# Kernel tuning notes

Hardware: AMD Instinct MI355X
Metric: run time of the kernel (lower is better)

Reference implementation:

```python
import jax, jax.numpy as jnp
import numpy as np

EPS = 1e-5


def _conv(x, w, b=None, pad=0):
    y = jax.lax.conv_general_dilated(
        x, w, window_strides=(1, 1), padding=[(pad, pad), (pad, pad)],
        dimension_numbers=('NCHW', 'OIHW', 'NCHW'))
    if b is not None:
        y = y + b[None, :, None, None]
    return y


def _bn(x, g, b, m, v):
    # eval-mode BatchNorm2d with running stats
    scale = (g / jnp.sqrt(v + EPS))[None, :, None, None]
    return (x - m[None, :, None, None]) * scale + b[None, :, None, None]


def setup_inputs() -> dict:
    key = jax.random.key(0)
    B, Ci, Cg, H, W = 4, 128, 64, 128, 128
    ks = iter(jax.random.split(key, 32))
    n = lambda shape, s=1.0: jax.random.normal(next(ks), shape, jnp.float32) * s
    return {
        'input': n((B, Ci, H, W)),
        'weight': n((B, Cg, H, W)),
        # conv11: 3x3, bias (norm_cfg=None) + ReLU
        'w11': n((Ci, Ci + Cg, 3, 3), 0.05), 'b11': n((Ci,), 0.05),
        # conv12: 1x1 -> Ci*9 per-pixel kernel generator
        'w12': n((Ci * 9, Ci, 1, 1), 0.05), 'b12': n((Ci * 9,), 0.05),
        # conv21: 3x3, bias + ReLU
        'w21': n((Ci, Ci + Cg, 3, 3), 0.05), 'b21': n((Ci,), 0.05),
        # conv22: 1x1 -> Ci*Ci channel-mix generator
        'w22': n((Ci * Ci, Ci, 1, 1), 0.05), 'b22': n((Ci * Ci,), 0.05),
        # BN after guided conv (self.local)
        'g1': 1.0 + n((Ci,), 0.1), 'be1': n((Ci,), 0.1), 'm1': n((Ci,), 0.1), 'v1': jnp.ones((Ci,), jnp.float32),
        # BN in self.br
        'g2': 1.0 + n((Ci,), 0.1), 'be2': n((Ci,), 0.1), 'm2': n((Ci,), 0.1), 'v2': jnp.ones((Ci,), jnp.float32),
        # conv3: 3x3 no bias (ConvModule with norm) + BN + ReLU
        'w3': n((Ci, Ci, 3, 3), 0.05),
        'g3': 1.0 + n((Ci,), 0.1), 'be3': n((Ci,), 0.1), 'm3': n((Ci,), 0.1), 'v3': jnp.ones((Ci,), jnp.float32),
    }


def _forward(input, weight, w11, b11, w12, b12, w21, b21, w22, b22,
             g1, be1, m1, v1, g2, be2, m2, v2, w3, g3, be3, m3, v3):
    B, Ci, H, W = input.shape
    wcat = jnp.concatenate([input, weight], axis=1)              # [B, Ci+Cg, H, W]
    w11o = jax.nn.relu(_conv(wcat, w11, b11, pad=1))             # [B, Ci, H, W]
    w12o = _conv(w11o, w12, b12, pad=0)                          # [B, Ci*9, H, W]
    w21o = jax.nn.relu(_conv(wcat, w21, b21, pad=1))             # [B, Ci, H, W]
    pooled = jnp.mean(w21o, axis=(2, 3), keepdims=True)          # [B, Ci, 1, 1]
    w22o = _conv(pooled, w22, b22, pad=0).reshape(B, Ci, Ci)     # [B, Ci, Ci]
    # Conv2dGuided: per-pixel 3x3 kernels from w12o applied depthwise
    xp = jnp.pad(input, ((0, 0), (0, 0), (1, 1), (1, 1)))
    patches = jnp.stack([xp[:, :, i:i + H, j:j + W]
                         for i in range(3) for j in range(3)], axis=2)  # [B, Ci, 9, H, W]
    local = jnp.sum(patches * w12o.reshape(B, Ci, 9, H, W), axis=2)     # [B, Ci, H, W]
    local = jax.nn.relu(_bn(local, g1, be1, m1, v1)).reshape(B, Ci, H * W)
    out = jnp.einsum('bij,bjn->bin', w22o, local).reshape(B, Ci, H, W)  # channel-mix bmm
    out = jax.nn.relu(_bn(out, g2, be2, m2, v2))                        # self.br
    out = jax.nn.relu(_bn(_conv(out, w3, None, pad=1), g3, be3, m3, v3))  # conv3
    return out


def reference(input, weight, w11, b11, w12, b12, w21, b21, w22, b22,
              g1, be1, m1, v1, g2, be2, m2, v2, w3, g3, be3, m3, v3):
    return _forward(input, weight, w11, b11, w12, b12, w21, b21, w22, b22,
                    g1, be1, m1, v1, g2, be2, m2, v2, w3, g3, be3, m3, v3)
```

## Files before the change

kernel.cpp:

```cpp
#include <hip/hip_runtime.h>
#include <math.h>

#define BB   4
#define CI   128
#define CG   64
#define CIN  192
#define HH   128
#define WW   128
#define PP   16384
#define EPSN 1e-5f

typedef unsigned short u16;
typedef unsigned int   u32;
typedef __attribute__((ext_vector_type(8))) short bf16x8;
typedef __attribute__((ext_vector_type(4))) float f32x4;

__device__ __forceinline__ u16 f2bf(float x) {
    union { float f; u32 u; } a; a.f = x;
    u32 u = a.u;
    return (u16)((u + 0x7FFFu + ((u >> 16) & 1u)) >> 16);
}
__device__ __forceinline__ float bf2f(u16 h) {
    union { u32 u; float f; } a; a.u = ((u32)h) << 16; return a.f;
}
__device__ __forceinline__ u32 swz(u32 o) { return o ^ ((o >> 4) & 0x70u); }

__device__ __forceinline__ void gld_lds16(const void* g, void* l) {
    __builtin_amdgcn_global_load_lds(
        (const __attribute__((address_space(1))) void*)g,
        (__attribute__((address_space(3))) void*)l, 16, 0, 0);
}

__global__ __launch_bounds__(256) void k_pack(
    const float* __restrict__ src0, int nch0,
    const float* __restrict__ src1, int nch1,
    u16* __restrict__ dhi, u16* __restrict__ dlo, int cinp)
{
    const int rr = blockIdx.x;
    const int b  = blockIdx.y;
    const int t  = threadIdx.x;
    u16* rh = dhi + ((size_t)b * 130 + rr) * 130 * cinp;
    u16* rl = dlo + ((size_t)b * 130 + rr) * 130 * cinp;

    if (rr == 0 || rr == 129) {
        u32* rh4 = (u32*)rh; u32* rl4 = (u32*)rl;
        const int tot = 130 * cinp / 2;
        for (int i = t; i < tot; i += 256) { rh4[i] = 0u; rl4[i] = 0u; }
        return;
    }
    const int y = rr - 1;
    for (int i = t; i < cinp; i += 256) {
        rh[i] = 0; rl[i] = 0;
        rh[129 * cinp + i] = 0; rl[129 * cinp + i] = 0;
    }

    __shared__ float xs[32][129];
    for (int ck = 0; ck < cinp / 32; ++ck) {
        __syncthreads();
        for (int i = t; i < 32 * 128; i += 256) {
            const int ch = i >> 7, col = i & 127;
            const int c = ck * 32 + ch;
            const float* sp = (c < nch0)
                ? src0 + ((size_t)b * nch0 + c) * PP
                : src1 + ((size_t)b * nch1 + (c - nch0)) * PP;
            xs[ch][col] = sp[y * WW + col];
        }
        __syncthreads();
        for (int i = t; i < 512; i += 256) {
            const int col = i >> 2, oct = i & 3;
            u16 hh[8], ll[8];
#pragma unroll
            for (int j = 0; j < 8; ++j) {
                const float v = xs[oct * 8 + j][col];
                const u16 h = f2bf(v);
                hh[j] = h; ll[j] = f2bf(v - bf2f(h));
            }
            const size_t off = (size_t)(col + 1) * cinp + ck * 32 + oct * 8;
            uint4 vh, vl;
            vh.x = (u32)hh[0] | ((u32)hh[1] << 16); vh.y = (u32)hh[2] | ((u32)hh[3] << 16);
            vh.z = (u32)hh[4] | ((u32)hh[5] << 16); vh.w = (u32)hh[6] | ((u32)hh[7] << 16);
            vl.x = (u32)ll[0] | ((u32)ll[1] << 16); vl.y = (u32)ll[2] | ((u32)ll[3] << 16);
            vl.z = (u32)ll[4] | ((u32)ll[5] << 16); vl.w = (u32)ll[6] | ((u32)ll[7] << 16);
            *(uint4*)(rh + off) = vh;
            *(uint4*)(rl + off) = vl;
        }
    }
}

__global__ __launch_bounds__(256) void k_wpack(
    const float* __restrict__ w0, const float* __restrict__ w1,
    u16* __restrict__ dst, int nmb, int nck, int cin)
{
    const int total = nmb * nck * 9 * 128 * 4;
    const int idx = blockIdx.x * 256 + threadIdx.x;
    if (idx >= total) return;
    const int oct = idx & 3; int r2 = idx >> 2;
    const int oc = r2 & 127; r2 >>= 7;
    const int tap = r2 % 9; r2 /= 9;
    const int ck = r2 % nck; r2 /= nck;
    const int mb = r2;
    const float* w = mb ? w1 : w0;
    u16 hh[8], ll[8];
#pragma unroll
    for (int j = 0; j < 8; ++j) {
        const int c = ck * 32 + oct * 8 + j;
        const float v = w[((size_t)oc * cin + c) * 9 + tap];
        const u16 h = f2bf(v);
        hh[j] = h; ll[j] = f2bf(v - bf2f(h));
    }
    const size_t halfs = (size_t)nmb * nck * 9 * 128 * 32;
    const size_t base = ((((size_t)mb * nck + ck) * 9 + tap) * 128 + oc) * 32 + oct * 8;
    uint4 vh, vl;
    vh.x = (u32)hh[0] | ((u32)hh[1] << 16); vh.y = (u32)hh[2] | ((u32)hh[3] << 16);
    vh.z = (u32)hh[4] | ((u32)hh[5] << 16); vh.w = (u32)hh[6] | ((u32)hh[7] << 16);
    vl.x = (u32)ll[0] | ((u32)ll[1] << 16); vl.y = (u32)ll[2] | ((u32)ll[3] << 16);
    vl.z = (u32)ll[4] | ((u32)ll[5] << 16); vl.w = (u32)ll[6] | ((u32)ll[7] << 16);
    *(uint4*)(dst + base) = vh;
    *(uint4*)(dst + halfs + base) = vl;
}

__global__ __launch_bounds__(256) void k_wpack12(
    const float* __restrict__ w12, u16* __restrict__ dst)
{
    const int idx = blockIdx.x * 256 + threadIdx.x;
    if (idx >= 18432) return;
    const int oct = idx & 15;
    const int g   = idx >> 4;
    const int cc  = g / 9, tap = g % 9;
    u16 hh[8], ll[8];
#pragma unroll
    for (int j = 0; j < 8; ++j) {
        const float v = w12[(size_t)g * 128 + oct * 8 + j];
        const u16 h = f2bf(v);
        hh[j] = h; ll[j] = f2bf(v - bf2f(h));
    }
    const size_t base = ((size_t)(tap * 128 + cc)) * 128 + oct * 8;
    uint4 vh, vl;
    vh.x = (u32)hh[0] | ((u32)hh[1] << 16); vh.y = (u32)hh[2] | ((u32)hh[3] << 16);
    vh.z = (u32)hh[4] | ((u32)hh[5] << 16); vh.w = (u32)hh[6] | ((u32)hh[7] << 16);
    vl.x = (u32)ll[0] | ((u32)ll[1] << 16); vl.y = (u32)ll[2] | ((u32)ll[3] << 16);
    vl.z = (u32)ll[4] | ((u32)ll[5] << 16); vl.w = (u32)ll[6] | ((u32)ll[7] << 16);
    *(uint4*)(dst + base) = vh;
    *(uint4*)(dst + 147456 + base) = vl;
}

template<int NCK, bool DUAL>
__global__ __launch_bounds__(256, 2) void k_conv_mfma(
    const u16* __restrict__ xhi, const u16* __restrict__ xlo,
    const u16* __restrict__ wA,
    const float* __restrict__ bias0, const float* __restrict__ bias1,
    const float* __restrict__ bng, const float* __restrict__ bnb,
    const float* __restrict__ bnm, const float* __restrict__ bnv,
    float* __restrict__ dst0, float* __restrict__ dst1,
    u16* __restrict__ y1ph, u16* __restrict__ y1pl)
{
    constexpr int CINP  = NCK * 32;
    constexpr int MBT   = DUAL ? 2 : 1;
    constexpr size_t WHALF = (size_t)MBT * NCK * 9 * 128 * 32;

    __shared__ char smem[73728];
    u16 (*Xs)[3][144][32] = (u16(*)[3][144][32])smem;
    u16 (*As)[128][32]    = (u16(*)[128][32])(smem + 55296);

    const int t    = threadIdx.x;
    const int wave = t >> 6;
    const int lane = t & 63;
    const int wm   = wave >> 1, wn = wave & 1;
    const int y    = blockIdx.x;
    const int mb   = blockIdx.y;
    const int b    = blockIdx.z;
    const int l15  = lane & 15;
    const int kg   = lane >> 4;

    f32x4 acc[4][4];
    if (DUAL) {
        const float* bp = mb ? bias1 : bias0;
#pragma unroll
        for (int fm = 0; fm < 4; ++fm) {
            const int ocb = wm * 64 + fm * 16 + kg * 4;
#pragma unroll
            for (int j = 0; j < 4; ++j) {
                const float bv = bp[ocb + j];
#pragma unroll
                for (int fn = 0; fn < 4; ++fn) acc[fm][fn][j] = bv;
            }
        }
    } else {
#pragma unroll
        for (int fm = 0; fm < 4; ++fm)
#pragma unroll
            for (int fn = 0; fn < 4; ++fn)
#pragma unroll
                for (int j = 0; j < 4; ++j) acc[fm][fn][j] = 0.0f;
    }

    const size_t xrow = (size_t)130 * CINP;

    for (int ck = 0; ck < NCK; ++ck) {
        __syncthreads();
        for (int idx = wave; idx < 54; idx += 4) {
            const int h = idx / 27, rem = idx % 27;
            const int r = rem / 9, iss = rem % 9;
            const u16* gb = (h ? xlo : xhi)
                + ((size_t)b * 130 + (y + r)) * xrow + ck * 32;
            const int o  = iss * 1024 + lane * 16;
            const int cc = o >> 6, rb = o & 63;
            gld_lds16((const char*)gb + (size_t)cc * (CINP * 2) + rb,
                      ((char*)&Xs[h][r][0][0]) + iss * 1024);
        }
        for (int tap = 0; tap < 9; ++tap) {
            for (int idx = wave; idx < 16; idx += 4) {
                const int h = idx >> 3, iss = idx & 7;
                const u16* gb = wA + (size_t)h * WHALF
                    + ((((size_t)mb * NCK + ck) * 9 + tap) * 128 * 32);
                gld_lds16((const char*)gb + iss * 1024 + lane * 16,
                          ((char*)&As[h][0][0]) + iss * 1024);
            }
            asm volatile("s_waitcnt vmcnt(0)" ::: "memory");
            __syncthreads();

            const int dy = tap / 3, dx = tap % 3;
            bf16x8 ah[4], al[4], bh[4], bl[4];
#pragma unroll
            for (int f = 0; f < 4; ++f) {
                const int row = wm * 64 + f * 16 + l15;
                ah[f] = *(const bf16x8*)&As[0][row][kg * 8];
                al[f] = *(const bf16x8*)&As[1][row][kg * 8];
                const int cc = wn * 64 + f * 16 + l15 + dx;
                bh[f] = *(const bf16x8*)&Xs[0][dy][cc][kg * 8];
                bl[f] = *(const bf16x8*)&Xs[1][dy][cc][kg * 8];
            }
#pragma unroll
            for (int fm = 0; fm < 4; ++fm)
#pragma unroll
                for (int fn = 0; fn < 4; ++fn) {
                    acc[fm][fn] = __builtin_amdgcn_mfma_f32_16x16x32_bf16(
                        al[fm], bh[fn], acc[fm][fn], 0, 0, 0);
                    acc[fm][fn] = __builtin_amdgcn_mfma_f32_16x16x32_bf16(
                        ah[fm], bl[fn], acc[fm][fn], 0, 0, 0);
                    acc[fm][fn] = __builtin_amdgcn_mfma_f32_16x16x32_bf16(
                        ah[fm], bh[fn], acc[fm][fn], 0, 0, 0);
                }
            __syncthreads();
        }
    }

    if (DUAL && mb == 0) {
        u16* img = (u16*)smem;
#pragma unroll
        for (int fm = 0; fm < 4; ++fm)
#pragma unroll
            for (int fn = 0; fn < 4; ++fn) {
                const int px = wn * 64 + fn * 16 + l15;
                const int c0 = wm * 64 + fm * 16 + kg * 4;
                u16 hh[4], ll[4];
#pragma unroll
                for (int j = 0; j < 4; ++j) {
                    const float v = fmaxf(acc[fm][fn][j], 0.0f);
                    const u16 h = f2bf(v);
                    hh[j] = h; ll[j] = f2bf(v - bf2f(h));
                }
                const u32 off = swz((u32)(px * 256 + c0 * 2));
                uint2 vh, vl;
                vh.x = (u32)hh[0] | ((u32)hh[1] << 16); vh.y = (u32)hh[2] | ((u32)hh[3] << 16);
                vl.x = (u32)ll[0] | ((u32)ll[1] << 16); vl.y = (u32)ll[2] | ((u32)ll[3] << 16);
                *(uint2*)((char*)img + off)         = vh;
                *(uint2*)((char*)img + 32768 + off) = vl;
            }
        __syncthreads();
        for (int h = 0; h < 2; ++h) {
            uint4* gd = (uint4*)((h ? y1pl : y1ph) + ((size_t)b * 128 + y) * 16384);
            const uint4* s4 = (const uint4*)(smem + h * 32768);
            for (int i = t; i < 2048; i += 256) gd[i] = s4[i];
        }
        return;
    }

    float* dst = DUAL ? dst1 : dst0;
#pragma unroll
    for (int fm = 0; fm < 4; ++fm) {
#pragma unroll
        for (int j = 0; j < 4; ++j) {
            const int oc = wm * 64 + fm * 16 + kg * 4 + j;
            float sc = 1.0f, sh = 0.0f;
            if (!DUAL) {
                sc = bng[oc] * rsqrtf(bnv[oc] + EPSN);
                sh = bnb[oc] - bnm[oc] * sc;
            }
            const size_t obase = ((size_t)b * CI + oc) * PP + (size_t)y * WW;
#pragma unroll
            for (int fn = 0; fn < 4; ++fn) {
                const int px = wn * 64 + fn * 16 + l15;
                float v = acc[fm][fn][j];
                if (!DUAL) v = fmaf(v, sc, sh);
                dst[obase + px] = fmaxf(v, 0.0f);
            }
        }
    }
}

__global__ __launch_bounds__(256) void k_pool(
    const float* __restrict__ y2, float* __restrict__ pooled)
{
    const int c = blockIdx.x, b = blockIdx.y, t = threadIdx.x;
    const float* src = y2 + ((size_t)b * CI + c) * PP;
    float s = 0.0f;
    for (int i = t; i < PP; i += 256) s += src[i];
    __shared__ float red[256];
    red[t] = s;
    __syncthreads();
    for (int st = 128; st > 0; st >>= 1) {
        if (t < st) red[t] += red[t + st];
        __syncthreads();
    }
    if (t == 0) pooled[b * CI + c] = red[0] * (1.0f / PP);
}

__global__ __launch_bounds__(256) void k_w22(
    const float* __restrict__ w22, const float* __restrict__ b22,
    const float* __restrict__ pooled, u16* __restrict__ w22p)
{
    const int b = blockIdx.y;
    const int o = blockIdx.x * 256 + threadIdx.x;
    __shared__ float pl[CI];
    if (threadIdx.x < CI) pl[threadIdx.x] = pooled[b * CI + threadIdx.x];
    __syncthreads();
    const float4* wr = (const float4*)(w22 + (size_t)o * CI);
    float acc = b22[o];
#pragma unroll 8
    for (int c4 = 0; c4 < CI / 4; ++c4) {
        const float4 w = wr[c4];
        acc += w.x * pl[c4 * 4 + 0] + w.y * pl[c4 * 4 + 1] +
               w.z * pl[c4 * 4 + 2] + w.w * pl[c4 * 4 + 3];
    }
    const u16 h = f2bf(acc);
    w22p[(size_t)b * 16384 + o] = h;
    w22p[65536 + (size_t)b * 16384 + o] = f2bf(acc - bf2f(h));
}

__global__ __launch_bounds__(256, 2) void k_guided_mfma(
    const float* __restrict__ input,
    const u16* __restrict__ y1p,
    const u16* __restrict__ w12p,
    const float* __restrict__ b12,
    const float* __restrict__ g1, const float* __restrict__ be1,
    const float* __restrict__ m1, const float* __restrict__ v1,
    u16* __restrict__ locp)
{
    __shared__ char smem[65536];
    const int t = threadIdx.x;
    const int wave = t >> 6, lane = t & 63;
    const int wm = wave >> 1, wn = wave & 1;
    const int l15 = lane & 15, kg = lane >> 4;
    const int y = blockIdx.x, b = blockIdx.y;

    for (int h = 0; h < 2; ++h) {
        const u16* gb = y1p + (size_t)h * 8388608 + ((size_t)b * 128 + y) * 16384;
        for (int iss = wave; iss < 32; iss += 4)
            gld_lds16((const char*)gb + iss * 1024 + lane * 16,
                      smem + h * 32768 + iss * 1024);
    }
    asm volatile("s_waitcnt vmcnt(0)" ::: "memory");
    __syncthreads();

    f32x4 accL[4][4];
#pragma unroll
    for (int fm = 0; fm < 4; ++fm)
#pragma unroll
        for (int fn = 0; fn < 4; ++fn)
#pragma unroll
            for (int j = 0; j < 4; ++j) accL[fm][fn][j] = 0.0f;

    const float* xb = input + (size_t)b * CI * PP;

    for (int tap = 0; tap < 9; ++tap) {
        const int ry  = y + tap / 3 - 1;
        const int dxo = tap % 3 - 1;
        if ((unsigned)ry >= (unsigned)HH) continue;

        f32x4 accG[4][4];
#pragma unroll
        for (int fm = 0; fm < 4; ++fm) {
            float bv[4];
#pragma unroll
            for (int j = 0; j < 4; ++j)
                bv[j] = b12[(wm * 64 + fm * 16 + kg * 4 + j) * 9 + tap];
#pragma unroll
            for (int fn = 0; fn < 4; ++fn)
#pragma unroll
                for (int j = 0; j < 4; ++j) accG[fm][fn][j] = bv[j];
        }

#pragma unroll
        for (int ks = 0; ks < 4; ++ks) {
            bf16x8 bh[4], bl[4];
#pragma unroll
            for (int f = 0; f < 4; ++f) {
                const int px = wn * 64 + f * 16 + l15;
                const u32 bo = swz((u32)(px * 256 + ks * 64 + kg * 16));
                bh[f] = *(const bf16x8*)(smem + bo);
                bl[f] = *(const bf16x8*)(smem + 32768 + bo);
            }
#pragma unroll
            for (int fm = 0; fm < 4; ++fm) {
                const size_t ao = ((size_t)(tap * 128 + wm * 64 + fm * 16 + l15)) * 128
                                  + ks * 32 + kg * 8;
                const bf16x8 ah = *(const bf16x8*)(w12p + ao);
                const bf16x8 al = *(const bf16x8*)(w12p + 147456 + ao);
#pragma unroll
                for (int fn = 0; fn < 4; ++fn) {
                    accG[fm][fn] = __builtin_amdgcn_mfma_f32_16x16x32_bf16(
                        al, bh[fn], accG[fm][fn], 0, 0, 0);
                    accG[fm][fn] = __builtin_amdgcn_mfma_f32_16x16x32_bf16(
                        ah, bl[fn], accG[fm][fn], 0, 0, 0);
                    accG[fm][fn] = __builtin_amdgcn_mfma_f32_16x16x32_bf16(
                        ah, bh[fn], accG[fm][fn], 0, 0, 0);
                }
            }
        }

#pragma unroll
        for (int fm = 0; fm < 4; ++fm)
#pragma unroll
            for (int fn = 0; fn < 4; ++fn) {
                const int px = wn * 64 + fn * 16 + l15;
                const int rx = px + dxo;
                const bool okx = (unsigned)rx < (unsigned)WW;
                const float* xr = xb + (size_t)ry * WW + (okx ? rx : 0);
#pragma unroll
                for (int j = 0; j < 4; ++j) {
                    const int ci = wm * 64 + fm * 16 + kg * 4 + j;
                    const float xv = okx ? xr[(size_t)ci * PP] : 0.0f;
                    accL[fm][fn][j] = fmaf(accG[fm][fn][j], xv, accL[fm][fn][j]);
                }
            }
    }

    __syncthreads();
    u16* img = (u16*)smem;
#pragma unroll
    for (int fm = 0; fm < 4; ++fm) {
        float sc[4], sh[4];
#pragma unroll
        for (int j = 0; j < 4; ++j) {
            const int cc = wm * 64 + fm * 16 + kg * 4 + j;
            sc[j] = g1[cc] * rsqrtf(v1[cc] + EPSN);
            sh[j] = be1[cc] - m1[cc] * sc[j];
        }
#pragma unroll
        for (int fn = 0; fn < 4; ++fn) {
            const int px = wn * 64 + fn * 16 + l15;
            const int c0 = wm * 64 + fm * 16 + kg * 4;
            u16 hh[4], ll[4];
#pragma unroll
            for (int j = 0; j < 4; ++j) {
                const float v = fmaxf(fmaf(accL[fm][fn][j], sc[j], sh[j]), 0.0f);
                const u16 h = f2bf(v);
                hh[j] = h; ll[j] = f2bf(v - bf2f(h));
            }
            const u32 off = swz((u32)(px * 256 + c0 * 2));
            uint2 vh, vl;
            vh.x = (u32)hh[0] | ((u32)hh[1] << 16); vh.y = (u32)hh[2] | ((u32)hh[3] << 16);
            vl.x = (u32)ll[0] | ((u32)ll[1] << 16); vl.y = (u32)ll[2] | ((u32)ll[3] << 16);
            *(uint2*)((char*)img + off)         = vh;
            *(uint2*)((char*)img + 32768 + off) = vl;
        }
    }
    __syncthreads();
    for (int h = 0; h < 2; ++h) {
        uint4* gd = (uint4*)(locp + (size_t)h * 8388608 + ((size_t)b * 128 + y) * 16384);
        const uint4* s4 = (const uint4*)(smem + h * 32768);
        for (int i = t; i < 2048; i += 256) gd[i] = s4[i];
    }
}

__global__ __launch_bounds__(256, 2) void k_bmm_mfma(
    const u16* __restrict__ locp, const u16* __restrict__ w22p,
    const float* __restrict__ g2, const float* __restrict__ be2,
    const float* __restrict__ m2, const float* __restrict__ v2,
    u16* __restrict__ x3h, u16* __restrict__ x3l)
{
    __shared__ char smem[65536];
    const int t = threadIdx.x;
    const int wave = t >> 6, lane = t & 63;
    const int wm = wave >> 1, wn = wave & 1;
    const int l15 = lane & 15, kg = lane >> 4;
    const int y = blockIdx.x, b = blockIdx.y;

    for (int h = 0; h < 2; ++h) {
        const u16* gb = locp + (size_t)h * 8388608 + ((size_t)b * 128 + y) * 16384;
        for (int iss = wave; iss < 32; iss += 4)
            gld_lds16((const char*)gb + iss * 1024 + lane * 16,
                      smem + h * 32768 + iss * 1024);
    }
    asm volatile("s_waitcnt vmcnt(0)" ::: "memory");
    __syncthreads();

    f32x4 acc[4][4];
#pragma unroll
    for (int fm = 0; fm < 4; ++fm)
#pragma unroll
        for (int fn = 0; fn < 4; ++fn)
#pragma unroll
            for (int j = 0; j < 4; ++j) acc[fm][fn][j] = 0.0f;

#pragma unroll
    for (int ks = 0; ks < 4; ++ks) {
        bf16x8 bh[4], bl[4];
#pragma unroll
        for (int f = 0; f < 4; ++f) {
            const int px = wn * 64 + f * 16 + l15;
            const u32 bo = swz((u32)(px * 256 + ks * 64 + kg * 16));
            bh[f] = *(const bf16x8*)(smem + bo);
            bl[f] = *(const bf16x8*)(smem + 32768 + bo);
        }
#pragma unroll
        for (int fm = 0; fm < 4; ++fm) {
            const size_t ao = ((size_t)(b * 128 + wm * 64 + fm * 16 + l15)) * 128
                              + ks * 32 + kg * 8;
            const bf16x8 ah = *(const bf16x8*)(w22p + ao);
            const bf16x8 al = *(const bf16x8*)(w22p + 65536 + ao);
#pragma unroll
            for (int fn = 0; fn < 4; ++fn) {
                acc[fm][fn] = __builtin_amdgcn_mfma_f32_16x16x32_bf16(
                    al, bh[fn], acc[fm][fn], 0, 0, 0);
                acc[fm][fn] = __builtin_amdgcn_mfma_f32_16x16x32_bf16(
                    ah, bl[fn], acc[fm][fn], 0, 0, 0);
                acc[fm][fn] = __builtin_amdgcn_mfma_f32_16x16x32_bf16(
                    ah, bh[fn], acc[fm][fn], 0, 0, 0);
            }
        }
    }

    __syncthreads();
    u16* img = (u16*)smem;
#pragma unroll
    for (int fm = 0; fm < 4; ++fm) {
        float sc[4], sh[4];
#pragma unroll
        for (int j = 0; j < 4; ++j) {
            const int cc = wm * 64 + fm * 16 + kg * 4 + j;
            sc[j] = g2[cc] * rsqrtf(v2[cc] + EPSN);
            sh[j] = be2[cc] - m2[cc] * sc[j];
        }
#pragma unroll
        for (int fn = 0; fn < 4; ++fn) {
            const int px = wn * 64 + fn * 16 + l15;
            const int c0 = wm * 64 + fm * 16 + kg * 4;
            u16 hh[4], ll[4];
#pragma unroll
            for (int j = 0; j < 4; ++j) {
                const float v = fmaxf(fmaf(acc[fm][fn][j], sc[j], sh[j]), 0.0f);
                const u16 h = f2bf(v);
                hh[j] = h; ll[j] = f2bf(v - bf2f(h));
            }
            const u32 off = (u32)(px * 256 + c0 * 2);
            uint2 vh, vl;
            vh.x = (u32)hh[0] | ((u32)hh[1] << 16); vh.y = (u32)hh[2] | ((u32)hh[3] << 16);
            vl.x = (u32)ll[0] | ((u32)ll[1] << 16); vl.y = (u32)ll[2] | ((u32)ll[3] << 16);
            *(uint2*)((char*)img + off)         = vh;
            *(uint2*)((char*)img + 32768 + off) = vl;
        }
    }
    __syncthreads();
    for (int h = 0; h < 2; ++h) {
        uint4* gd = (uint4*)((h ? x3l : x3h)
            + (((size_t)b * 130 + y + 1) * 130 + 1) * 128);
        const uint4* s4 = (const uint4*)(smem + h * 32768);
        for (int i = t; i < 2048; i += 256) gd[i] = s4[i];
    }
}

__global__ __launch_bounds__(256) void k_zero3(u16* __restrict__ x3)
{
    const int idx = blockIdx.x * 256 + threadIdx.x;
    if (idx >= 264192) return;
    const int hb = idx / 33024;
    int r2 = idx % 33024;
    u32* base = (u32*)(x3 + (size_t)(hb >> 2) * 8652800
                          + (size_t)(hb & 3) * 130 * 130 * 128);
    if (r2 < 8320)            base[r2] = 0u;
    else if (r2 < 16640)      base[(size_t)129 * 8320 + (r2 - 8320)] = 0u;
    else {
        const int q = r2 - 16640;
        const int w = q & 63;
        const int r = q >> 6;
        const int row = 1 + (r >> 1);
        const int side = r & 1;
        base[(size_t)row * 8320 + (side ? 8256 : 0) + w] = 0u;
    }
}

extern "C" void kernel_launch(void* const* d_in, const int* in_sizes, int n_in,
                              void* d_out, int out_size, void* d_ws, size_t ws_size,
                              hipStream_t stream)
{
    (void)in_sizes; (void)n_in; (void)out_size; (void)ws_size;

    const float* input  = (const float*)d_in[0];
    const float* weight = (const float*)d_in[1];
    const float* w11    = (const float*)d_in[2];
    const float* b11    = (const float*)d_in[3];
    const float* w12    = (const float*)d_in[4];
    const float* b12    = (const float*)d_in[5];
    const float* w21    = (const float*)d_in[6];
    const float* b21    = (const float*)d_in[7];
    const float* w22    = (const float*)d_in[8];
    const float* b22    = (const float*)d_in[9];
    const float* g1     = (const float*)d_in[10];
    const float* be1    = (const float*)d_in[11];
    const float* m1     = (const float*)d_in[12];
    const float* v1     = (const float*)d_in[13];
    const float* g2     = (const float*)d_in[14];
    const float* be2    = (const float*)d_in[15];
    const float* m2     = (const float*)d_in[16];
    const float* v2     = (const float*)d_in[17];
    const float* w3     = (const float*)d_in[18];
    const float* g3     = (const float*)d_in[19];
    const float* be3    = (const float*)d_in[20];
    const float* m3     = (const float*)d_in[21];
    const float* v3     = (const float*)d_in[22];

    float* ws     = (float*)d_ws;
    float* y2o    = ws;
    float* pooled = ws + 8388608;
    u16*   w22p   = (u16*)(ws + 8389120);
    u16*   wAd    = (u16*)(ws + 8454656);
    u16*   wA3    = (u16*)(ws + 8897024);
    u16*   w12p   = (u16*)(ws + 9044480);
    u16*   xpadDh = (u16*)(ws + 9191936);
    u16*   xpadDl = xpadDh + 12979200;
    u16*   locp   = (u16*)(ws + 9191936);
    u16*   y1p    = (u16*)(ws + 22171136);
    u16*   x3h    = (u16*)(ws + 22171136);
    u16*   x3l    = x3h + 8652800;
    float* outp   = (float*)d_out;

    k_pack<<<dim3(130, BB), 256, 0, stream>>>(input, CI, weight, CG, xpadDh, xpadDl, CIN);
    k_wpack<<<dim3(216), 256, 0, stream>>>(w11, w21, wAd, 2, 6, CIN);
    k_wpack<<<dim3(72), 256, 0, stream>>>(w3, w3, wA3, 1, 4, CI);
    k_wpack12<<<dim3(72), 256, 0, stream>>>(w12, w12p);

    k_conv_mfma<6, true><<<dim3(128, 2, BB), 256, 0, stream>>>(
        xpadDh, xpadDl, wAd, b11, b21, nullptr, nullptr, nullptr, nullptr,
        nullptr, y2o, y1p, y1p + 8388608);

    k_pool<<<dim3(CI, BB), 256, 0, stream>>>(y2o, pooled);
    k_w22<<<dim3(64, BB), 256, 0, stream>>>(w22, b22, pooled, w22p);

    k_guided_mfma<<<dim3(128, BB), 256, 0, stream>>>(
        input, y1p, w12p, b12, g1, be1, m1, v1, locp);

    k_zero3<<<dim3(1032), 256, 0, stream>>>(x3h);

    k_bmm_mfma<<<dim3(128, BB), 256, 0, stream>>>(
        locp, w22p, g2, be2, m2, v2, x3h, x3l);

    k_conv_mfma<4, false><<<dim3(128, 1, BB), 256, 0, stream>>>(
        x3h, x3l, wA3, nullptr, nullptr, g3, be3, m3, v3, outp, nullptr,
        nullptr, nullptr);
}
```

Measured before the change: 577.2 us.

## Load conv weights directly from global, swizzle input LDS tile, remap row order

```diff
diff --git a/kernel.cpp b/kernel.cpp
--- a/kernel.cpp
+++ b/kernel.cpp
@@ -24,11 +24,15 @@
     union { u32 u; float f; } a; a.u = ((u32)h) << 16; return a.f;
 }
 __device__ __forceinline__ u32 swz(u32 o) { return o ^ ((o >> 4) & 0x70u); }
+__device__ __forceinline__ int xslot(int cc) { return (cc >> 1) & 3; }
 
 __device__ __forceinline__ void gld_lds16(const void* g, void* l) {
     __builtin_amdgcn_global_load_lds(
         (const __attribute__((address_space(1))) void*)g,
         (__attribute__((address_space(3))) void*)l, 16, 0, 0);
+}
+__device__ __forceinline__ int yswz(int bid) {
+    return ((bid & 7) << 4) | (bid >> 3);
 }
 
 __global__ __launch_bounds__(256) void k_pack(
@@ -158,15 +162,13 @@
     constexpr int MBT   = DUAL ? 2 : 1;
     constexpr size_t WHALF = (size_t)MBT * NCK * 9 * 128 * 32;
 
-    __shared__ char smem[73728];
-    u16 (*Xs)[3][144][32] = (u16(*)[3][144][32])smem;
-    u16 (*As)[128][32]    = (u16(*)[128][32])(smem + 55296);
+    __shared__ char smem[65536];
 
     const int t    = threadIdx.x;
     const int wave = t >> 6;
     const int lane = t & 63;
     const int wm   = wave >> 1, wn = wave & 1;
-    const int y    = blockIdx.x;
+    const int y    = yswz(blockIdx.x);
     const int mb   = blockIdx.y;
     const int b    = blockIdx.z;
     const int l15  = lane & 15;
@@ -203,32 +205,27 @@
             const int r = rem / 9, iss = rem % 9;
             const u16* gb = (h ? xlo : xhi)
                 + ((size_t)b * 130 + (y + r)) * xrow + ck * 32;
-            const int o  = iss * 1024 + lane * 16;
-            const int cc = o >> 6, rb = o & 63;
+            const int cc = iss * 16 + (lane >> 2);
+            const int rb = ((lane & 3) << 4) ^ (xslot(cc) << 4);
             gld_lds16((const char*)gb + (size_t)cc * (CINP * 2) + rb,
-                      ((char*)&Xs[h][r][0][0]) + iss * 1024);
-        }
+                      smem + (h * 3 + r) * 9216 + iss * 1024);
+        }
+        asm volatile("s_waitcnt vmcnt(0)" ::: "memory");
+        __syncthreads();
+
         for (int tap = 0; tap < 9; ++tap) {
-            for (int idx = wave; idx < 16; idx += 4) {
-                const int h = idx >> 3, iss = idx & 7;
-                const u16* gb = wA + (size_t)h * WHALF
-                    + ((((size_t)mb * NCK + ck) * 9 + tap) * 128 * 32);
-                gld_lds16((const char*)gb + iss * 1024 + lane * 16,
-                          ((char*)&As[h][0][0]) + iss * 1024);
-            }
-            asm volatile("s_waitcnt vmcnt(0)" ::: "memory");
-            __syncthreads();
-
             const int dy = tap / 3, dx = tap % 3;
+            const size_t abase = (((size_t)mb * NCK + ck) * 9 + tap) * 4096;
             bf16x8 ah[4], al[4], bh[4], bl[4];
 #pragma unroll
             for (int f = 0; f < 4; ++f) {
-                const int row = wm * 64 + f * 16 + l15;
-                ah[f] = *(const bf16x8*)&As[0][row][kg * 8];
-                al[f] = *(const bf16x8*)&As[1][row][kg * 8];
+                const size_t ao = abase + (size_t)(wm * 64 + f * 16 + l15) * 32 + kg * 8;
+                ah[f] = *(const bf16x8*)(wA + ao);
+                al[f] = *(const bf16x8*)(wA + WHALF + ao);
                 const int cc = wn * 64 + f * 16 + l15 + dx;
-                bh[f] = *(const bf16x8*)&Xs[0][dy][cc][kg * 8];
-                bl[f] = *(const bf16x8*)&Xs[1][dy][cc][kg * 8];
+                const char* bp0 = smem + dy * 9216 + cc * 64 + ((kg ^ xslot(cc)) << 4);
+                bh[f] = *(const bf16x8*)bp0;
+                bl[f] = *(const bf16x8*)(bp0 + 27648);
             }
 #pragma unroll
             for (int fm = 0; fm < 4; ++fm)
@@ -241,11 +238,11 @@
                     acc[fm][fn] = __builtin_amdgcn_mfma_f32_16x16x32_bf16(
                         ah[fm], bh[fn], acc[fm][fn], 0, 0, 0);
                 }
-            __syncthreads();
         }
     }
 
     if (DUAL && mb == 0) {
+        __syncthreads();
         u16* img = (u16*)smem;
 #pragma unroll
         for (int fm = 0; fm < 4; ++fm)
@@ -352,7 +349,7 @@
     const int wave = t >> 6, lane = t & 63;
     const int wm = wave >> 1, wn = wave & 1;
     const int l15 = lane & 15, kg = lane >> 4;
-    const int y = blockIdx.x, b = blockIdx.y;
+    const int y = yswz(blockIdx.x), b = blockIdx.y;
 
     for (int h = 0; h < 2; ++h) {
         const u16* gb = y1p + (size_t)h * 8388608 + ((size_t)b * 128 + y) * 16384;
```

Measured after the change: 577.7 us. Within noise of the previous version (+0.1%).
